# Kernel optimization log

Measured on AMD Instinct MI355X. Metric: run time of the kernel, lower is better.

Reference implementation:

```python
import jax, jax.numpy as jnp
import numpy as np

B, S, V, E, H = 256, 512, 800, 128, 256

def setup_inputs() -> dict:
    key = jax.random.key(0)
    ks = jax.random.split(key, 16)
    def rn(k, shape, scale=0.05):
        return jax.random.normal(k, shape, dtype=jnp.float32) * scale
    return {
        "x": jax.random.randint(ks[0], (B, S), 0, V),
        "emb": rn(ks[1], (V, E), 1.0),
        "Wih0": rn(ks[2], (4 * H, E)),
        "Whh0": rn(ks[3], (4 * H, H)),
        "bih0": rn(ks[4], (4 * H,)),
        "bhh0": rn(ks[5], (4 * H,)),
        "Wih1": rn(ks[6], (4 * H, H)),
        "Whh1": rn(ks[7], (4 * H, H)),
        "bih1": rn(ks[8], (4 * H,)),
        "bhh1": rn(ks[9], (4 * H,)),
        "ln_g": jnp.ones((H,), jnp.float32),
        "ln_b": jnp.zeros((H,), jnp.float32),
        "proj_W": rn(ks[10], (E, H)),
        "proj_b": rn(ks[11], (E,)),
    }

def _lstm_layer(x, Wih, Whh, bih, bhh):
    # x: [B, S, D]; returns full hidden sequence [B, S, H]
    b, s, _ = x.shape
    h0 = jnp.zeros((b, H), x.dtype)
    c0 = jnp.zeros((b, H), x.dtype)
    # precompute input projections for all timesteps: [S, B, 4H]
    xp = jnp.einsum("bsd,gd->sbg", x, Wih) + bih + bhh

    def step(carry, xp_t):
        h, c = carry
        gates = xp_t + h @ Whh.T  # [B, 4H]
        i, f, g, o = jnp.split(gates, 4, axis=-1)  # torch gate order i,f,g,o
        i = jax.nn.sigmoid(i)
        f = jax.nn.sigmoid(f)
        g = jnp.tanh(g)
        o = jax.nn.sigmoid(o)
        c = f * c + i * g
        h = o * jnp.tanh(c)
        return (h, c), h

    (_, _), hs = jax.lax.scan(step, (h0, c0), xp)
    return hs.transpose(1, 0, 2)  # [B, S, H]

def reference(x, emb, Wih0, Whh0, bih0, bhh0, Wih1, Whh1, bih1, bhh1, ln_g, ln_b, proj_W, proj_b):
    table = emb.at[0].set(0.0)  # padding_idx=0
    e = table[x]  # [B, S, E]
    h1 = _lstm_layer(e, Wih0, Whh0, bih0, bhh0)
    h2 = _lstm_layer(h1, Wih1, Whh1, bih1, bhh1)
    hn = h2[:, -1, :]  # h_n[-1]: last layer, final timestep [B, H]
    mu = jnp.mean(hn, axis=-1, keepdims=True)
    var = jnp.mean(jnp.square(hn - mu), axis=-1, keepdims=True)
    y = (hn - mu) * jax.lax.rsqrt(var + 1e-5) * ln_g + ln_b
    return y @ proj_W.T + proj_b  # [B, 128]
```

## Files before the change

### kernel.cpp

```cpp
#include <hip/hip_runtime.h>
#include <hip/hip_bf16.h>


typedef unsigned short u16;
typedef unsigned int   u32;
using short8 = __attribute__((ext_vector_type(8))) short;
using f32x4  = __attribute__((ext_vector_type(4))) float;

#define NB 256
#define NS 512
#define NE 128
#define NH 256
#define NG 1024

#define WLDS_FRAGS 18
#define HOFF 147456
#define SCAN_LDS (HOFF + 2 * 16 * NH * 2)

#define NSCAN 32
#define NHELP 96
#define NWG   (NSCAN + NHELP)

#define L2E     1.4426950408889634f
#define TWO_L2E 2.8853900817779268f

__device__ __forceinline__ u16 f2b(float x) {
  __hip_bfloat16 h = __float2bfloat16(x);
  return __builtin_bit_cast(u16, h);
}
__device__ __forceinline__ float b2f(u16 u) {
  return __builtin_bit_cast(float, (u32)u << 16);
}
__device__ __forceinline__ float ex2(float x)  { return __builtin_amdgcn_exp2f(x); }
__device__ __forceinline__ float ex2n(float x) { return __builtin_amdgcn_exp2f(-x); }
__device__ __forceinline__ float rcpa(float x) { return __builtin_amdgcn_rcpf(x); }

__device__ __forceinline__ void gbar(u32* bar, int ph, int tid, int bid) {
  __syncthreads();
  if (tid == 0) {
    __threadfence();
    __hip_atomic_fetch_add(bar + (bid & 7) * 32, 1u,
                           __ATOMIC_RELAXED, __HIP_MEMORY_SCOPE_AGENT);
  }
  if (tid < 64) {
    u32 target = (u32)NWG * (u32)(ph + 1);
    for (;;) {
      u32 v = 0;
      if (tid < 8)
        v = __hip_atomic_load(bar + tid * 32, __ATOMIC_RELAXED,
                              __HIP_MEMORY_SCOPE_AGENT);
      v += __shfl_down(v, 4);
      v += __shfl_down(v, 2);
      v += __shfl_down(v, 1);
      v = __shfl(v, 0);
      if (v >= target) break;
      __builtin_amdgcn_s_sleep(8);
    }
  }
  __syncthreads();
  if (tid == 0) __threadfence();
  __syncthreads();
}

__global__ __launch_bounds__(256) void prep_weights(
    const float* Wih0, const float* Whh0, const float* bih0, const float* bhh0,
    const float* Wih1, const float* Whh1, const float* bih1, const float* bhh1,
    u16* wih0b, u16* whh0b, u16* wih1b, u16* whh1b, float* bc0, float* bc1) {
  int stride = gridDim.x * blockDim.x;
  int tid = blockIdx.x * blockDim.x + threadIdx.x;
  for (int i = tid; i < NG * NE; i += stride) {
    float s = (((i >> 7) >> 8) == 2) ? TWO_L2E : L2E;
    wih0b[i] = f2b(Wih0[i] * s);
  }
  for (int i = tid; i < NG * NH; i += stride) {
    float s = (((i >> 8) >> 8) == 2) ? TWO_L2E : L2E;
    whh0b[i] = f2b(Whh0[i] * s);
    wih1b[i] = f2b(Wih1[i] * s);
    whh1b[i] = f2b(Whh1[i] * s);
  }
  for (int i = tid; i < NG; i += stride) {
    float s = ((i >> 8) == 2) ? TWO_L2E : L2E;
    bc0[i] = (bih0[i] + bhh0[i]) * s;
    bc1[i] = (bih1[i] + bhh1[i]) * s;
  }
}

__global__ __launch_bounds__(256) void zero_flags(u32* f, int n) {
  int i = blockIdx.x * 256 + threadIdx.x;
  if (i < n) f[i] = 0;
}

__global__ __launch_bounds__(256) void embed_chunk(const int* __restrict__ x,
                                                   const float* __restrict__ emb,
                                                   u16* __restrict__ ebuf, int t0) {
  int gid = blockIdx.x * 256 + threadIdx.x;
  int d4 = gid & 31;
  int sb = gid >> 5;
  int b  = sb & (NB - 1);
  int sl = sb >> 8;
  int tok = x[b * NS + (t0 + sl)];
  float4 v = make_float4(0.f, 0.f, 0.f, 0.f);
  if (tok != 0) v = *(const float4*)(emb + (size_t)tok * NE + d4 * 4);
  ushort4 o;
  o.x = f2b(v.x); o.y = f2b(v.y); o.z = f2b(v.z); o.w = f2b(v.w);
  *(ushort4*)(ebuf + (size_t)sb * NE + d4 * 4) = o;
}

template <int K>
__global__ __launch_bounds__(256) void xp_gemm(const u16* __restrict__ A,
                                               const u16* __restrict__ W,
                                               const float* __restrict__ bias,
                                               u16* __restrict__ Cout) {
  __shared__ __align__(16) char lds[2 * 128 * 80];
  char* Asm = lds;
  char* Bsm = lds + 128 * 80;
  int tid = threadIdx.x;
  int w = tid >> 6, l = tid & 63;
  int hi = l >> 4, lo = l & 15;
  int mblk = blockIdx.x >> 3, nblk = blockIdx.x & 7;
  size_t arow0 = (size_t)mblk * 128;
  int g0 = nblk * 128;
  int wm = (w >> 1) * 64, wn = (w & 1) * 64;
  f32x4 acc[4][4] = {};
  int r = tid >> 1, cp = tid & 1;

  for (int k0 = 0; k0 < K; k0 += 32) {
    int4 a0 = *(const int4*)(A + (arow0 + r) * K + k0 + cp * 16);
    int4 a1 = *(const int4*)(A + (arow0 + r) * K + k0 + cp * 16 + 8);
    int4 b0 = *(const int4*)(W + (size_t)(g0 + r) * K + k0 + cp * 16);
    int4 b1 = *(const int4*)(W + (size_t)(g0 + r) * K + k0 + cp * 16 + 8);
    *(int4*)(Asm + r * 80 + cp * 32)      = a0;
    *(int4*)(Asm + r * 80 + cp * 32 + 16) = a1;
    *(int4*)(Bsm + r * 80 + cp * 32)      = b0;
    *(int4*)(Bsm + r * 80 + cp * 32 + 16) = b1;
    __syncthreads();
    short8 af[4], bfr[4];
#pragma unroll
    for (int mt = 0; mt < 4; ++mt)
      af[mt] = *(const short8*)(Asm + (wm + mt * 16 + lo) * 80 + hi * 16);
#pragma unroll
    for (int nt = 0; nt < 4; ++nt)
      bfr[nt] = *(const short8*)(Bsm + (wn + nt * 16 + lo) * 80 + hi * 16);
#pragma unroll
    for (int mt = 0; mt < 4; ++mt)
#pragma unroll
      for (int nt = 0; nt < 4; ++nt)
        acc[mt][nt] = __builtin_amdgcn_mfma_f32_16x16x32_bf16(af[mt], bfr[nt], acc[mt][nt], 0, 0, 0);
    __syncthreads();
  }
#pragma unroll
  for (int nt = 0; nt < 4; ++nt) {
    int gc = g0 + wn + nt * 16 + lo;
    float bv = bias[gc];
    int ws_ = (gc >> 4) & 7, mts = gc >> 7, his = (gc >> 2) & 3, rs = gc & 3;
    size_t gbase = ((size_t)(ws_ * 8 + mts) << 8) + (size_t)(his * 16) * 4 + rs;
#pragma unroll
    for (int mt = 0; mt < 4; ++mt) {
      size_t row = arow0 + wm + mt * 16 + hi * 4;
#pragma unroll
      for (int rr = 0; rr < 4; ++rr) {
        size_t rw = row + rr;
        int t = (int)(rw >> 8), ba = (int)(rw & 255);
        size_t e = ((size_t)(t * 16 + (ba >> 4)) << 14) + gbase + (size_t)(ba & 15) * 4;
        Cout[e] = f2b(acc[mt][nt][rr] + bv);
      }
    }
  }
}

__global__ __launch_bounds__(512, 2)
void lstm_persist(const int* __restrict__ x, const float* __restrict__ emb,
                  const u16* __restrict__ wih0b, const float* __restrict__ bc0,
                  const u16* __restrict__ whh0b, const u16* __restrict__ whh1b,
                  const u16* __restrict__ wih1b, const float* __restrict__ bc1,
                  u16* __restrict__ xpA0, u16* __restrict__ xpA1,
                  u16* __restrict__ xpB0, u16* __restrict__ xpB1,
                  u16* __restrict__ io0, u16* __restrict__ io1,
                  float* __restrict__ hs1, u32* __restrict__ bar,
                  int T, int nch) {
  extern __shared__ __align__(16) char smem[];
  int bid = blockIdx.x;
  int tid = threadIdx.x;

  if (bid >= NSCAN) {
    int team = tid >> 8, tt = tid & 255;
    char* Asm = smem + team * 40960;
    char* Bsm = Asm + 20480;
    int wq = tt >> 6, lq = tt & 63;
    int hiq = lq >> 4, loq = lq & 15;
    int wm = (wq >> 1) * 64, wn = (wq & 1) * 64;
    int r = tt >> 1, cp = tt & 1;
    int tg = (bid - NSCAN) * 2 + team;
    const int stride = NHELP * 2;
    int njobs = T * 16;
    int nIt = (njobs + stride - 1) / stride;

    for (int s = 0; s <= nch + 1; ++s) {
      if (s + 1 < nch) {
        u16* xpC = ((s + 1) & 1) ? xpA1 : xpA0;
        int t0c = (s + 1) * T;
        for (int it = 0; it < nIt; ++it) {
          int j = tg + it * stride;
          bool act = j < njobs;
          int jj = act ? j : 0;
          int mblk = jj >> 3, nblk = jj & 7;
          size_t arow0 = (size_t)mblk * 128;
          int g0 = nblk * 128;
          f32x4 acc[4][4] = {};
          int rw = (int)(arow0 + r);
          int sl = rw >> 8, ba = rw & 255;
          int tok = x[ba * NS + t0c + sl];
          const float* erow = emb + (size_t)tok * NE;
          for (int k0 = 0; k0 < NE; k0 += 32) {
            const float* src = erow + k0 + cp * 16;
            u32 pk[8];
#pragma unroll
            for (int q = 0; q < 8; ++q) {
              float a = src[2 * q], b = src[2 * q + 1];
              if (tok == 0) { a = 0.0f; b = 0.0f; }
              pk[q] = (u32)f2b(a) | ((u32)f2b(b) << 16);
            }
            *(int4*)(Asm + r * 80 + cp * 32)      = *(int4*)&pk[0];
            *(int4*)(Asm + r * 80 + cp * 32 + 16) = *(int4*)&pk[4];
            int4 b0 = *(const int4*)(wih0b + (size_t)(g0 + r) * NE + k0 + cp * 16);
            int4 b1 = *(const int4*)(wih0b + (size_t)(g0 + r) * NE + k0 + cp * 16 + 8);
            *(int4*)(Bsm + r * 80 + cp * 32)      = b0;
            *(int4*)(Bsm + r * 80 + cp * 32 + 16) = b1;
            __syncthreads();
            short8 af[4], bfr[4];
#pragma unroll
            for (int mt = 0; mt < 4; ++mt)
              af[mt] = *(const short8*)(Asm + (wm + mt * 16 + loq) * 80 + hiq * 16);
#pragma unroll
            for (int nt = 0; nt < 4; ++nt)
              bfr[nt] = *(const short8*)(Bsm + (wn + nt * 16 + loq) * 80 + hiq * 16);
#pragma unroll
            for (int mt = 0; mt < 4; ++mt)
#pragma unroll
              for (int nt = 0; nt < 4; ++nt)
                acc[mt][nt] = __builtin_amdgcn_mfma_f32_16x16x32_bf16(af[mt], bfr[nt], acc[mt][nt], 0, 0, 0);
            __syncthreads();
          }
          if (act) {
#pragma unroll
            for (int nt = 0; nt < 4; ++nt) {
              int gc = g0 + wn + nt * 16 + loq;
              float bv = bc0[gc];
              int ws_ = (gc >> 4) & 7, mts = gc >> 7, his = (gc >> 2) & 3, rs = gc & 3;
              size_t gbase = ((size_t)(ws_ * 8 + mts) << 8) + (size_t)(his * 16) * 4 + rs;
#pragma unroll
              for (int mt = 0; mt < 4; ++mt) {
                size_t row = arow0 + wm + mt * 16 + hiq * 4;
#pragma unroll
                for (int rr = 0; rr < 4; ++rr) {
                  size_t rw2 = row + rr;
                  int t = (int)(rw2 >> 8), ba2 = (int)(rw2 & 255);
                  size_t e = ((size_t)(t * 16 + (ba2 >> 4)) << 14) + gbase + (size_t)(ba2 & 15) * 4;
                  xpC[e] = f2b(acc[mt][nt][rr] + bv);
                }
              }
            }
          }
        }
      }
      if (s >= 1 && s <= nch) {
        const u16* hsrc = ((s - 1) & 1) ? io1 : io0;
        u16* xdst = ((s - 1) & 1) ? xpB1 : xpB0;
        for (int it = 0; it < nIt; ++it) {
          int j = tg + it * stride;
          bool act = j < njobs;
          int jj = act ? j : 0;
          int mblk = jj >> 3, nblk = jj & 7;
          size_t arow0 = (size_t)mblk * 128;
          int g0 = nblk * 128;
          f32x4 acc[4][4] = {};
          for (int k0 = 0; k0 < NH; k0 += 32) {
            int4 a0 = *(const int4*)(hsrc + (arow0 + r) * NH + k0 + cp * 16);
            int4 a1 = *(const int4*)(hsrc + (arow0 + r) * NH + k0 + cp * 16 + 8);
            int4 b0 = *(const int4*)(wih1b + (size_t)(g0 + r) * NH + k0 + cp * 16);
            int4 b1 = *(const int4*)(wih1b + (size_t)(g0 + r) * NH + k0 + cp * 16 + 8);
            *(int4*)(Asm + r * 80 + cp * 32)      = a0;
            *(int4*)(Asm + r * 80 + cp * 32 + 16) = a1;
            *(int4*)(Bsm + r * 80 + cp * 32)      = b0;
            *(int4*)(Bsm + r * 80 + cp * 32 + 16) = b1;
            __syncthreads();
            short8 af[4], bfr[4];
#pragma unroll
            for (int mt = 0; mt < 4; ++mt)
              af[mt] = *(const short8*)(Asm + (wm + mt * 16 + loq) * 80 + hiq * 16);
#pragma unroll
            for (int nt = 0; nt < 4; ++nt)
              bfr[nt] = *(const short8*)(Bsm + (wn + nt * 16 + loq) * 80 + hiq * 16);
#pragma unroll
            for (int mt = 0; mt < 4; ++mt)
#pragma unroll
              for (int nt = 0; nt < 4; ++nt)
                acc[mt][nt] = __builtin_amdgcn_mfma_f32_16x16x32_bf16(af[mt], bfr[nt], acc[mt][nt], 0, 0, 0);
            __syncthreads();
          }
          if (act) {
#pragma unroll
            for (int nt = 0; nt < 4; ++nt) {
              int gc = g0 + wn + nt * 16 + loq;
              float bv = bc1[gc];
              int ws_ = (gc >> 4) & 7, mts = gc >> 7, his = (gc >> 2) & 3, rs = gc & 3;
              size_t gbase = ((size_t)(ws_ * 8 + mts) << 8) + (size_t)(his * 16) * 4 + rs;
#pragma unroll
              for (int mt = 0; mt < 4; ++mt) {
                size_t row = arow0 + wm + mt * 16 + hiq * 4;
#pragma unroll
                for (int rr = 0; rr < 4; ++rr) {
                  size_t rw2 = row + rr;
                  int t = (int)(rw2 >> 8), ba2 = (int)(rw2 & 255);
                  size_t e = ((size_t)(t * 16 + (ba2 >> 4)) << 14) + gbase + (size_t)(ba2 & 15) * 4;
                  xdst[e] = f2b(acc[mt][nt][rr] + bv);
                }
              }
            }
          }
        }
      }
      if (s <= nch) gbar(bar, s, tid, bid);
    }
    return;
  }

  int roleB = bid >> 4;
  int bgi = bid & 15;
  int bg = bgi * 16;
  const u16* whh = roleB ? whh1b : whh0b;

  int w = tid >> 6, l = tid & 63;
  int hi = l >> 4, lo = l & 15;

  int wbase = w * (WLDS_FRAGS * 1024) + l * 16;
  short8 wfv[8][5];
  short8 wfv2[6];
#pragma unroll
  for (int mt = 0; mt < 8; ++mt) {
#pragma unroll
    for (int p = 0; p < 8; ++p) {
      const u16* src = whh + (size_t)(16 * (w + 8 * mt) + lo) * NH + p * 32 + hi * 8;
      short8 v = *(const short8*)src;
      if (p < 2)                 *(short8*)(smem + wbase + (p * 8 + mt) * 1024) = v;
      else if (p == 2 && mt < 2) *(short8*)(smem + wbase + (16 + mt) * 1024) = v;
      else if (p == 2)           wfv2[mt - 2] = v;
      else                       wfv[mt][p - 3] = v;
    }
  }
  float c[2][4];
  for (int i = tid; i < 16 * NH / 2; i += 512) ((u32*)(smem + HOFF))[i] = 0;
#pragma unroll
  for (int g = 0; g < 2; ++g)
#pragma unroll
    for (int r = 0; r < 4; ++r) c[g][r] = 0.0f;
  __syncthreads();

  int rdoff = (l ^ ((l >> 3) & 7)) * 16;
  int wroff[2];
#pragma unroll
  for (int g = 0; g < 2; ++g) {
    int xx = (2 * (w & 1) + (hi >> 1)) * 16 + lo;
    wroff[g] = (4 * g + (w >> 1)) * 1024 + (xx ^ ((xx >> 3) & 7)) * 16 + 8 * (hi & 1);
  }
  int bq = tid >> 5, kc = tid & 31;
  int xw = (kc & 3) * 16 + bq;
  int wboff = (kc >> 2) * 1024 + (xw ^ ((xw >> 3) & 7)) * 16;
  size_t wb_glob = (size_t)(bg + bq) * NH + kc * 8;

  f32x4 acc[8];
  for (int s = 0; s <= nch + 1; ++s) {
    bool act = roleB ? (s >= 2) : (s < nch);
    if (act) {
      int mc = roleB ? (s - 2) : s;
      const u16* xp = roleB ? ((mc & 1) ? xpB1 : xpB0)
                            : ((mc & 1) ? xpA1 : xpA0);
      u16* hout = roleB ? (u16*)0 : ((s & 1) ? io1 : io0);
      const u16* xpp = xp + ((size_t)(bgi * 8 + w) * 2048) + (size_t)l * 4;
      ushort4 xq[8];
#pragma unroll
      for (int mt = 0; mt < 8; ++mt) xq[mt] = *(const ushort4*)(xpp + mt * 256);

      for (int t = 0; t < T; ++t) {
        int rbase = HOFF + ((t & 1) << 13);
        int wbbase = HOFF + ((~t & 1) << 13);
#pragma unroll
        for (int mt = 0; mt < 8; ++mt) {
          f32x4 a;
          a[0] = b2f(xq[mt].x); a[1] = b2f(xq[mt].y);
          a[2] = b2f(xq[mt].z); a[3] = b2f(xq[mt].w);
          acc[mt] = a;
        }
        xpp += 262144;
#pragma unroll
        for (int mt = 0; mt < 8; ++mt) xq[mt] = *(const ushort4*)(xpp + mt * 256);
#pragma unroll
        for (int p = 0; p < 8; ++p) {
          short8 bf = *(const short8*)(smem + rbase + rdoff + p * 1024);
#pragma unroll
          for (int mt = 0; mt < 8; ++mt) {
            short8 af;
            if (p < 2)                 af = *(const short8*)(smem + wbase + (p * 8 + mt) * 1024);
            else if (p == 2 && mt < 2) af = *(const short8*)(smem + wbase + (16 + mt) * 1024);
            else if (p == 2)           af = wfv2[mt - 2];
            else                       af = wfv[mt][p - 3];
            acc[mt] = __builtin_amdgcn_mfma_f32_16x16x32_bf16(af, bf, acc[mt], 0, 0, 0);
          }
        }
#pragma unroll
        for (int g = 0; g < 2; ++g) {
          float hv[4];
#pragma unroll
          for (int r = 0; r < 4; ++r) {
            float iv = rcpa(1.0f + ex2n(acc[g][r]));
            float fv = rcpa(1.0f + ex2n(acc[2 + g][r]));
            float gv = 1.0f - 2.0f * rcpa(ex2(acc[4 + g][r]) + 1.0f);
            float ov = rcpa(1.0f + ex2n(acc[6 + g][r]));
            float cc = fv * c[g][r] + iv * gv;
            c[g][r] = cc;
            float th = 1.0f - 2.0f * rcpa(ex2(cc * TWO_L2E) + 1.0f);
            hv[r] = ov * th;
          }
          u32 d0, d1;
          asm("v_cvt_pk_bf16_f32 %0, %1, %2" : "=v"(d0) : "v"(hv[0]), "v"(hv[1]));
          asm("v_cvt_pk_bf16_f32 %0, %1, %2" : "=v"(d1) : "v"(hv[2]), "v"(hv[3]));
          uint2 hw; hw.x = d0; hw.y = d1;
          *(uint2*)(smem + wbbase + wroff[g]) = hw;
        }
        __syncthreads();
        if (hout) {
          int4 hv4 = *(const int4*)(smem + wbbase + wboff);
          *(int4*)(hout + wb_glob + ((size_t)t << 16)) = hv4;
        }
      }
    }
    if (s <= nch) gbar(bar, s, tid, bid);
  }

  if (roleB) {
#pragma unroll
    for (int g = 0; g < 2; ++g) {
      ushort4 hv4 = *(const ushort4*)(smem + HOFF + wroff[g]);
      int j = 16 * w + 128 * g + 4 * hi;
      u16 hb[4] = {hv4.x, hv4.y, hv4.z, hv4.w};
#pragma unroll
      for (int r = 0; r < 4; ++r)
        hs1[(size_t)(bg + lo) * NH + j + r] = b2f(hb[r]);
    }
  }
}

__global__ __launch_bounds__(256) void ln_proj(const float* __restrict__ hn,
                                               const float* __restrict__ lng,
                                               const float* __restrict__ lnb,
                                               const float* __restrict__ pW,
                                               const float* __restrict__ pb,
                                               float* __restrict__ out) {
  __shared__ __align__(16) float nbuf[NH];
  __shared__ float red[8];
  int b = blockIdx.x, tid = threadIdx.x;
  float v = hn[(size_t)b * NH + tid];
  float s = v, s2 = v * v;
#pragma unroll
  for (int o = 32; o > 0; o >>= 1) {
    s  += __shfl_down(s, o);
    s2 += __shfl_down(s2, o);
  }
  if ((tid & 63) == 0) { red[tid >> 6] = s; red[4 + (tid >> 6)] = s2; }
  __syncthreads();
  if (tid == 0) {
    red[0] = red[0] + red[1] + red[2] + red[3];
    red[4] = red[4] + red[5] + red[6] + red[7];
  }
  __syncthreads();
  float mean = red[0] * (1.0f / NH);
  float var  = red[4] * (1.0f / NH) - mean * mean;
  float rs = rsqrtf(var + 1e-5f);
  nbuf[tid] = (v - mean) * rs * lng[tid] + lnb[tid];
  __syncthreads();
  if (tid < NE) {
    float a = pb[tid];
    const float* wr = pW + (size_t)tid * NH;
#pragma unroll 4
    for (int j = 0; j < NH; ++j) a = fmaf(nbuf[j], wr[j], a);
    out[(size_t)b * NE + tid] = a;
  }
}

extern "C" void kernel_launch(void* const* d_in, const int* in_sizes, int n_in,
                              void* d_out, int out_size, void* d_ws, size_t ws_size,
                              hipStream_t stream) {
  const int*   x     = (const int*)d_in[0];
  const float* emb   = (const float*)d_in[1];
  const float* Wih0  = (const float*)d_in[2];
  const float* Whh0  = (const float*)d_in[3];
  const float* bih0  = (const float*)d_in[4];
  const float* bhh0  = (const float*)d_in[5];
  const float* Wih1  = (const float*)d_in[6];
  const float* Whh1  = (const float*)d_in[7];
  const float* bih1  = (const float*)d_in[8];
  const float* bhh1  = (const float*)d_in[9];
  const float* ln_g  = (const float*)d_in[10];
  const float* ln_b  = (const float*)d_in[11];
  const float* projW = (const float*)d_in[12];
  const float* projb = (const float*)d_in[13];

  hipFuncSetAttribute((const void*)lstm_persist,
                      hipFuncAttributeMaxDynamicSharedMemorySize, SCAN_LDS);

  const size_t FIXED = 2400256;
  int T = 64;
  while (T > 4 && FIXED + (size_t)T * 2359296 > ws_size) T >>= 1;
  int nch = NS / T;

  char* ws = (char*)d_ws;
  u16*   xpA0  = (u16*)(ws);
  u16*   xpA1  = (u16*)(ws + (size_t)T * 524288);
  u16*   xpB0  = (u16*)(ws + (size_t)T * 1048576);
  u16*   xpB1  = (u16*)(ws + (size_t)T * 1572864);
  u16*   io0   = (u16*)(ws + (size_t)T * 2097152);
  u16*   io1   = (u16*)(ws + (size_t)T * 2228224);
  char*  wbase = ws + (size_t)T * 2359296;
  u16*   wih0b = (u16*)(wbase);
  u16*   whh0b = (u16*)(wbase + 262144);
  u16*   wih1b = (u16*)(wbase + 786432);
  u16*   whh1b = (u16*)(wbase + 1310720);
  float* bc0   = (float*)(wbase + 1835008);
  float* bc1   = (float*)(wbase + 1839104);
  float* hs1   = (float*)(wbase + 1843200);
  u32*   bar   = (u32*)(wbase + 2105344);

  zero_flags<<<4, 256, 0, stream>>>(bar, 1024);
  prep_weights<<<256, 256, 0, stream>>>(Wih0, Whh0, bih0, bhh0, Wih1, Whh1, bih1, bhh1,
                                        wih0b, whh0b, wih1b, whh1b, bc0, bc1);
  embed_chunk<<<T * 32, 256, 0, stream>>>(x, emb, xpB0, 0);
  xp_gemm<NE><<<T * 16, 256, 0, stream>>>(xpB0, wih0b, bc0, xpA0);

  lstm_persist<<<NWG, 512, SCAN_LDS, stream>>>(
      x, emb, wih0b, bc0, whh0b, whh1b, wih1b, bc1,
      xpA0, xpA1, xpB0, xpB1, io0, io1, hs1, bar, T, nch);

  ln_proj<<<NB, 256, 0, stream>>>(hs1, ln_g, ln_b, projW, projb, (float*)d_out);
}
```

Before: 1.392 ms.

## Replace global grid barrier with producer-consumer counters between scan and helper groups

The all-workgroup phase barrier is replaced by three monotonic counters: scan-A, scan-B and the helper GEMM workgroups each signal their own counter, and each role waits only on the counters it actually depends on. Idle iterations are dropped from the scan loops. This is meant to cut the cost of every workgroup waiting on all others each chunk, and to let the two layers and the helpers drift relative to each other. It risks ordering and visibility bugs in the counter targets and fences. It also relies on a single thread polling one counter instead of the spread-out barrier slots.

```diff
diff --git a/kernel.cpp b/kernel.cpp
--- a/kernel.cpp
+++ b/kernel.cpp
@@ -35,30 +35,20 @@
 __device__ __forceinline__ float ex2n(float x) { return __builtin_amdgcn_exp2f(-x); }
 __device__ __forceinline__ float rcpa(float x) { return __builtin_amdgcn_rcpf(x); }
 
-__device__ __forceinline__ void gbar(u32* bar, int ph, int tid, int bid) {
+__device__ __forceinline__ void sigCtr(u32* c, int tid, bool rel) {
   __syncthreads();
   if (tid == 0) {
+    if (rel) __threadfence();
+    __hip_atomic_fetch_add(c, 1u, __ATOMIC_RELAXED, __HIP_MEMORY_SCOPE_AGENT);
+  }
+}
+__device__ __forceinline__ void waitCtr(u32* c, int target, int tid) {
+  if (target <= 0) return;
+  if (tid == 0) {
+    while ((int)__hip_atomic_load(c, __ATOMIC_RELAXED, __HIP_MEMORY_SCOPE_AGENT) < target)
+      __builtin_amdgcn_s_sleep(4);
     __threadfence();
-    __hip_atomic_fetch_add(bar + (bid & 7) * 32, 1u,
-                           __ATOMIC_RELAXED, __HIP_MEMORY_SCOPE_AGENT);
-  }
-  if (tid < 64) {
-    u32 target = (u32)NWG * (u32)(ph + 1);
-    for (;;) {
-      u32 v = 0;
-      if (tid < 8)
-        v = __hip_atomic_load(bar + tid * 32, __ATOMIC_RELAXED,
-                              __HIP_MEMORY_SCOPE_AGENT);
-      v += __shfl_down(v, 4);
-      v += __shfl_down(v, 2);
-      v += __shfl_down(v, 1);
-      v = __shfl(v, 0);
-      if (v >= target) break;
-      __builtin_amdgcn_s_sleep(8);
-    }
-  }
-  __syncthreads();
-  if (tid == 0) __threadfence();
+  }
   __syncthreads();
 }
 
@@ -181,6 +171,9 @@
   extern __shared__ __align__(16) char smem[];
   int bid = blockIdx.x;
   int tid = threadIdx.x;
+  u32* CA = bar;
+  u32* CB = bar + 32;
+  u32* CH = bar + 64;
 
   if (bid >= NSCAN) {
     int team = tid >> 8, tt = tid & 255;
@@ -195,7 +188,8 @@
     int njobs = T * 16;
     int nIt = (njobs + stride - 1) / stride;
 
-    for (int s = 0; s <= nch + 1; ++s) {
+    for (int s = 0; s <= nch; ++s) {
+      waitCtr(CA, 16 * s, tid);
       if (s + 1 < nch) {
         u16* xpC = ((s + 1) & 1) ? xpA1 : xpA0;
         int t0c = (s + 1) * T;
@@ -263,7 +257,8 @@
           }
         }
       }
-      if (s >= 1 && s <= nch) {
+      waitCtr(CB, 16 * (s - 2), tid);
+      if (s >= 1) {
         const u16* hsrc = ((s - 1) & 1) ? io1 : io0;
         u16* xdst = ((s - 1) & 1) ? xpB1 : xpB0;
         for (int it = 0; it < nIt; ++it) {
@@ -320,7 +315,7 @@
           }
         }
       }
-      if (s <= nch) gbar(bar, s, tid, bid);
+      sigCtr(CH, tid, true);
     }
     return;
   }
@@ -369,9 +364,11 @@
   size_t wb_glob = (size_t)(bg + bq) * NH + kc * 8;
 
   f32x4 acc[8];
-  for (int s = 0; s <= nch + 1; ++s) {
-    bool act = roleB ? (s >= 2) : (s < nch);
-    if (act) {
+  int s0 = roleB ? 2 : 0;
+  int s1 = roleB ? (nch + 1) : (nch - 1);
+  for (int s = s0; s <= s1; ++s) {
+    waitCtr(CH, 96 * s, tid);
+    {
       int mc = roleB ? (s - 2) : s;
       const u16* xp = roleB ? ((mc & 1) ? xpB1 : xpB0)
                             : ((mc & 1) ? xpA1 : xpA0);
@@ -434,7 +431,7 @@
         }
       }
     }
-    if (s <= nch) gbar(bar, s, tid, bid);
+    sigCtr(roleB ? CB : CA, tid, !roleB);
   }
 
   if (roleB) {
```

Result: no change. 1.369 ms (-1.6%).
